# Performance work log

Measured on AMD Instinct MI355X. Metric: run time of the kernel, lower is better.

The kernel has to match this reference:

```python
import jax, jax.numpy as jnp
import numpy as np

B, S, D, HD, H = 4, 4096, 1024, 120, 1  # batch, seq, d_model, h_dim, heads (code only runs for h=1)
EPS = 1e-12  # F.normalize eps


def setup_inputs() -> dict:
    key = jax.random.key(0)
    k0, k1, k2, k3 = jax.random.split(key, 4)
    query = jax.random.normal(k0, (B, S, D), dtype=jnp.float32)
    key_t = jax.random.normal(k1, (B, S, D), dtype=jnp.float32)  # unused by forward, but a required arg
    # q_linear: Linear(d_model, h_dim*h) -> weight [HD, D], bias [HD]
    Wq = jax.random.normal(k2, (HD * H, D), dtype=jnp.float32) * np.float32(1.0 / np.sqrt(D))
    bq = jnp.zeros((HD * H,), dtype=jnp.float32)
    # weight_tensor: xavier_uniform on shape (h, d_k) = (1, 120)
    bound = np.float32(np.sqrt(6.0 / (H + HD * H)))
    weight_tensor = jax.random.uniform(k3, (H, HD * H), dtype=jnp.float32, minval=-bound, maxval=bound)
    return {"query": query, "key": key_t, "Wq": Wq, "bq": bq, "weight_tensor": weight_tensor}


def reference(query, key, Wq, bq, weight_tensor):
    # context = q_linear(query).view(B, -1, h_dim); with h=1 this is [B, S, HD]
    context = jnp.einsum('bsd,hd->bsh', query, Wq) + bq  # [B,S,HD]
    # context_fc = context.unsqueeze(0) * weight_tensor[h,1,1,d_k] -> [h,B,S,HD]
    ctx = context[None, :, :, :] * weight_tensor[:, None, None, :]  # [h,B,S,HD]
    # F.normalize(p=2, dim=-1): x / max(||x||, eps)
    nrm = jnp.sqrt(jnp.sum(ctx * ctx, axis=-1, keepdims=True))
    ctx_n = ctx / jnp.maximum(nrm, EPS)
    # per-head gram matrix then mean over heads -> [B,S,S]
    scores = jnp.einsum('hbsd,hbtd->hbst', ctx_n, ctx_n).mean(axis=0)
    # mask=None path; dropout is identity in eval mode
    return jax.nn.softmax(scores, axis=-1)
```

## Files before the change

kernel.cpp:

```cpp
#include <hip/hip_runtime.h>
#include <hip/hip_fp16.h>

#define BATCH   4
#define SEQ     4096
#define DMODEL  1024
#define HDIM    120
#define ROWS_TOTAL (BATCH * SEQ)
#define TPB     256

typedef float f32x4 __attribute__((ext_vector_type(4)));
typedef short s16x8 __attribute__((ext_vector_type(8)));

#define FRAG_PER_B ((size_t)TPB * 4 * 64)

static __device__ __forceinline__ unsigned short f2bf(float f) {
    unsigned u = __float_as_uint(f);
    u += 0x7FFFu + ((u >> 16) & 1u);
    return (unsigned short)(u >> 16);
}
static __device__ __forceinline__ s16x8 pack2x4(f32x4 lo, f32x4 hi) {
    s16x8 r;
#pragma unroll
    for (int i = 0; i < 4; ++i) r[i] = (short)f2bf(lo[i]);
#pragma unroll
    for (int i = 0; i < 4; ++i) r[4 + i] = (short)f2bf(hi[i]);
    return r;
}

__global__ __launch_bounds__(64)
void wq_frag_kernel(const float* __restrict__ Wq, const float* __restrict__ wt,
                    s16x8* __restrict__ WF)
{
    const int lane = threadIdx.x;
    const int l15  = lane & 15;
    const int l4   = lane >> 4;
    const int ct   = blockIdx.x >> 5;
    const int ks   = blockIdx.x & 31;
    const int col  = ct * 16 + l15;

    f32x4 lo = (f32x4){0.f,0.f,0.f,0.f}, hi = lo;
    if (col < HDIM) {
        const float w = wt[col];
        const float* src = Wq + (size_t)col * DMODEL + ks * 32 + l4 * 8;
        lo = *(const f32x4*)(src);
        hi = *(const f32x4*)(src + 4);
#pragma unroll
        for (int i = 0; i < 4; ++i) { lo[i] *= w; hi[i] *= w; }
    }
    WF[((size_t)(ct * 32 + ks)) * 64 + lane] = pack2x4(lo, hi);
}

__global__ __launch_bounds__(512)
void ctx_norm_kernel(const float* __restrict__ query,
                     const s16x8* __restrict__ WF,
                     const float* __restrict__ bq,
                     const float* __restrict__ wt,
                     s16x8* __restrict__ F)
{
    __shared__ unsigned short lA[2][64 * 40];
    __shared__ float lsq[64][2];
    __shared__ unsigned short lt[64][136];

    const int tid  = threadIdx.x;
    const int lane = tid & 63;
    const int wv   = tid >> 6;
    const int wr   = wv & 3;
    const int wc   = wv >> 2;
    const int l15  = lane & 15;
    const int l4   = lane >> 4;
    const int row0 = blockIdx.x * 64;

    const int arow = tid >> 3, achk = tid & 7;
    const float* aload = query + (size_t)(row0 + arow) * DMODEL + achk * 4;

    f32x4 acc[4];
#pragma unroll
    for (int n = 0; n < 4; ++n) acc[n] = (f32x4){0.f,0.f,0.f,0.f};

    f32x4 pr = *(const f32x4*)(aload);
    {
        const unsigned u0 = (unsigned)f2bf(pr[0]) | ((unsigned)f2bf(pr[1]) << 16);
        const unsigned u1 = (unsigned)f2bf(pr[2]) | ((unsigned)f2bf(pr[3]) << 16);
        *(uint2*)&lA[0][arow * 40 + achk * 4] = make_uint2(u0, u1);
    }

    for (int ks = 0; ks < 32; ++ks) {
        __syncthreads();
        if (ks + 1 < 32) pr = *(const f32x4*)(aload + (ks + 1) * 32);
        const int buf = ks & 1;
        const s16x8 a = *(const s16x8*)&lA[buf][(wr * 16 + l15) * 40 + l4 * 8];
#pragma unroll
        for (int n = 0; n < 4; ++n) {
            const s16x8 bfr = WF[((size_t)((wc * 4 + n) * 32 + ks)) * 64 + lane];
            acc[n] = __builtin_amdgcn_mfma_f32_16x16x32_bf16(a, bfr, acc[n], 0, 0, 0);
        }
        if (ks + 1 < 32) {
            const unsigned u0 = (unsigned)f2bf(pr[0]) | ((unsigned)f2bf(pr[1]) << 16);
            const unsigned u1 = (unsigned)f2bf(pr[2]) | ((unsigned)f2bf(pr[3]) << 16);
            *(uint2*)&lA[buf ^ 1][arow * 40 + achk * 4] = make_uint2(u0, u1);
        }
    }

    float sumsq[4] = {0.f,0.f,0.f,0.f};
#pragma unroll
    for (int n = 0; n < 4; ++n) {
        const int col = wc * 64 + n * 16 + l15;
        const float bqv = (col < HDIM) ? bq[col] * wt[col] : 0.f;
#pragma unroll
        for (int r = 0; r < 4; ++r) {
            const float v = acc[n][r] + bqv;
            acc[n][r] = v;
            sumsq[r] += v * v;
        }
    }
#pragma unroll
    for (int r = 0; r < 4; ++r) {
        float s = sumsq[r];
        s += __shfl_xor(s, 1);
        s += __shfl_xor(s, 2);
        s += __shfl_xor(s, 4);
        s += __shfl_xor(s, 8);
        sumsq[r] = s;
    }
    if (l15 == 0) {
#pragma unroll
        for (int r = 0; r < 4; ++r)
            lsq[wr * 16 + l4 * 4 + r][wc] = sumsq[r];
    }
    __syncthreads();
#pragma unroll
    for (int r = 0; r < 4; ++r) {
        const int lr = wr * 16 + l4 * 4 + r;
        const float s = lsq[lr][0] + lsq[lr][1];
        const float rinv = 1.f / fmaxf(sqrtf(s), 1e-12f);
#pragma unroll
        for (int n = 0; n < 4; ++n)
            lt[lr][wc * 64 + n * 16 + l15] = f2bf(acc[n][r] * rinv);
    }
    __syncthreads();
#pragma unroll
    for (int q = 0; q < 2; ++q) {
        const int idx = wv * 2 + q;
        const int tl  = idx >> 2;
        const int k4  = idx & 3;
        const s16x8 fr = *(const s16x8*)&lt[tl * 16 + l15][k4 * 32 + l4 * 8];
        F[((size_t)(blockIdx.x * 4 + tl) * 4 + k4) * 64 + lane] = fr;
    }
}

#define LOADT5(dst, t) { const s16x8* _p = base + (size_t)(t) * 2048;          \
    dst[0] = _p[0]; dst[1] = _p[64]; dst[2] = _p[128]; dst[3] = _p[192]; }

#define COMPT5(src, t) { f32x4 _a = (f32x4){0.f, 0.f, 0.f, 0.f};               \
    _a = __builtin_amdgcn_mfma_f32_16x16x32_bf16(src[0], rfrag[0], _a, 0,0,0); \
    _a = __builtin_amdgcn_mfma_f32_16x16x32_bf16(src[1], rfrag[1], _a, 0,0,0); \
    _a = __builtin_amdgcn_mfma_f32_16x16x32_bf16(src[2], rfrag[2], _a, 0,0,0); \
    _a = __builtin_amdgcn_mfma_f32_16x16x32_bf16(src[3], rfrag[3], _a, 0,0,0); \
    const float _e0 = __expf(_a[0]), _e1 = __expf(_a[1]);                      \
    const float _e2 = __expf(_a[2]), _e3 = __expf(_a[3]);                      \
    rs += (_e0 + _e1) + (_e2 + _e3);                                           \
    const __half2 _h01 = __floats2half2_rn(_e0, _e1);                          \
    const __half2 _h23 = __floats2half2_rn(_e2, _e3);                          \
    ex0[t] = *(const unsigned*)&_h01;                                          \
    ex1[t] = *(const unsigned*)&_h23; }

__global__ __launch_bounds__(512, 4)
void gram_fused_kernel(const s16x8* __restrict__ F, float* __restrict__ out)
{
    __shared__ unsigned short lsB[16 * 1024];
    __shared__ float lsum[16][8];

    const int tid  = threadIdx.x;
    const int lane = tid & 63;
    const int cg   = tid >> 6;
    const int l15  = lane & 15;
    const int l4   = lane >> 4;
    char* lsb = (char*)&lsB[0];

    const int u    = ((blockIdx.x & 7) << 7) | (blockIdx.x >> 3);
    const int b    = u >> 8;
    const int tr   = u & 255;
    const s16x8* Fb = F + (size_t)b * FRAG_PER_B;

    s16x8 rfrag[4];
#pragma unroll
    for (int ks = 0; ks < 4; ++ks) rfrag[ks] = Fb[((size_t)tr * 4 + ks) * 64 + lane];

    const s16x8* base = Fb + (size_t)cg * 256 + lane;

    unsigned ex0[32], ex1[32];
    float rs = 0.f;
    s16x8 cf[4];

#pragma unroll
    for (int t = 0; t < 32; ++t) {
        LOADT5(cf, t)
        COMPT5(cf, t)
    }

    rs += __shfl_xor(rs, 16);
    rs += __shfl_xor(rs, 32);
    if (lane < 16) lsum[lane][cg] = rs;
    __syncthreads();

    const int r0 = cg * 2, r1 = cg * 2 + 1;
    float s0 = 0.f, s1 = 0.f;
#pragma unroll
    for (int w = 0; w < 8; ++w) { s0 += lsum[r0][w]; s1 += lsum[r1][w]; }
    const float rv0 = 1.f / s0;
    const float rv1 = 1.f / s1;

    float* ob0 = out + ((size_t)b * SEQ + tr * 16 + r0) * SEQ;
    float* ob1 = out + ((size_t)b * SEQ + tr * 16 + r1) * SEQ;
    const unsigned wswz = (unsigned)((l15 & 7) << 4);
    const unsigned rswz0 = (unsigned)((r0 & 7) << 4);
    const unsigned rswz1 = (unsigned)((r1 & 7) << 4);

#pragma unroll
    for (int c = 0; c < 4; ++c) {
        if (c > 0) __syncthreads();
#pragma unroll
        for (int i = 0; i < 8; ++i) {
            const int t = c * 8 + i;
            const unsigned byte = ((unsigned)(l15 * 2048 + (i * 8 + cg) * 32 + l4 * 8)) ^ wswz;
            *(uint2*)(lsb + byte) = make_uint2(ex0[t], ex1[t]);
        }
        __syncthreads();
#pragma unroll
        for (int it = 0; it < 4; ++it) {
            const unsigned byA = ((unsigned)(r0 * 2048 + it * 512 + lane * 8)) ^ rswz0;
            const uint2 dA = *(const uint2*)(lsb + byA);
            const float2 a01 = __half22float2(*(const __half2*)&dA.x);
            const float2 a23 = __half22float2(*(const __half2*)&dA.y);
            f32x4 pA;
            pA[0] = a01.x * rv0; pA[1] = a01.y * rv0;
            pA[2] = a23.x * rv0; pA[3] = a23.y * rv0;
            __builtin_nontemporal_store(pA, (f32x4*)(ob0 + c * 1024 + it * 256 + lane * 4));

            const unsigned byB = ((unsigned)(r1 * 2048 + it * 512 + lane * 8)) ^ rswz1;
            const uint2 dB = *(const uint2*)(lsb + byB);
            const float2 b01 = __half22float2(*(const __half2*)&dB.x);
            const float2 b23 = __half22float2(*(const __half2*)&dB.y);
            f32x4 pB;
            pB[0] = b01.x * rv1; pB[1] = b01.y * rv1;
            pB[2] = b23.x * rv1; pB[3] = b23.y * rv1;
            __builtin_nontemporal_store(pB, (f32x4*)(ob1 + c * 1024 + it * 256 + lane * 4));
        }
    }
}

extern "C" void kernel_launch(void* const* d_in, const int* in_sizes, int n_in,
                              void* d_out, int out_size, void* d_ws, size_t ws_size,
                              hipStream_t stream)
{
    const float* query = (const float*)d_in[0];
    const float* Wq    = (const float*)d_in[2];
    const float* bq    = (const float*)d_in[3];
    const float* wt    = (const float*)d_in[4];
    float* out = (float*)d_out;
    s16x8* F  = (s16x8*)d_ws;
    s16x8* WF = (s16x8*)((char*)d_ws + (size_t)4 * 1024 * 1024);

    wq_frag_kernel<<<dim3(256), dim3(64), 0, stream>>>(Wq, wt, WF);
    ctx_norm_kernel<<<dim3(ROWS_TOTAL / 64), dim3(512), 0, stream>>>(query, WF, bq, wt, F);
    gram_fused_kernel<<<dim3(BATCH * TPB), dim3(512), 0, stream>>>(F, out);
}
```

Measured before the change: 120.1 us.

## Split fused gram-softmax into rowsum pass and double-buffered recompute-and-stream pass

The single fused kernel, which held all exponentials in registers before writing, is replaced by two kernels. The first computes row sums of exp(scores) for 32-row groups and stores the reciprocals. The second recomputes the gram tiles with MFMA and exponentiates them into a double-buffered LDS staging area, overlapping the next chunk's compute with the current chunk's nontemporal output stores. The aim is to cut register pressure and overlap compute with the dominant output write, at the cost of computing the gram matrix twice, one extra launch, and larger LDS use per block.

```diff
diff --git a/kernel.cpp b/kernel.cpp
--- a/kernel.cpp
+++ b/kernel.cpp
@@ -148,88 +148,139 @@
     }
 }
 
-#define LOADT5(dst, t) { const s16x8* _p = base + (size_t)(t) * 2048;          \
-    dst[0] = _p[0]; dst[1] = _p[64]; dst[2] = _p[128]; dst[3] = _p[192]; }
-
-#define COMPT5(src, t) { f32x4 _a = (f32x4){0.f, 0.f, 0.f, 0.f};               \
-    _a = __builtin_amdgcn_mfma_f32_16x16x32_bf16(src[0], rfrag[0], _a, 0,0,0); \
-    _a = __builtin_amdgcn_mfma_f32_16x16x32_bf16(src[1], rfrag[1], _a, 0,0,0); \
-    _a = __builtin_amdgcn_mfma_f32_16x16x32_bf16(src[2], rfrag[2], _a, 0,0,0); \
-    _a = __builtin_amdgcn_mfma_f32_16x16x32_bf16(src[3], rfrag[3], _a, 0,0,0); \
-    const float _e0 = __expf(_a[0]), _e1 = __expf(_a[1]);                      \
-    const float _e2 = __expf(_a[2]), _e3 = __expf(_a[3]);                      \
-    rs += (_e0 + _e1) + (_e2 + _e3);                                           \
-    const __half2 _h01 = __floats2half2_rn(_e0, _e1);                          \
-    const __half2 _h23 = __floats2half2_rn(_e2, _e3);                          \
-    ex0[t] = *(const unsigned*)&_h01;                                          \
-    ex1[t] = *(const unsigned*)&_h23; }
-
 __global__ __launch_bounds__(512, 4)
-void gram_fused_kernel(const s16x8* __restrict__ F, float* __restrict__ out)
-{
-    __shared__ unsigned short lsB[16 * 1024];
-    __shared__ float lsum[16][8];
+void rowsum_kernel(const s16x8* __restrict__ F, float* __restrict__ rinv)
+{
+    __shared__ float lsum[32][8];
 
     const int tid  = threadIdx.x;
     const int lane = tid & 63;
     const int cg   = tid >> 6;
     const int l15  = lane & 15;
+
+    const int u    = ((blockIdx.x & 7) << 6) | (blockIdx.x >> 3);
+    const int b    = u >> 7;
+    const int rg   = u & 127;
+    const s16x8* Fb = F + (size_t)b * FRAG_PER_B;
+
+    s16x8 rfA[4], rfB[4];
+#pragma unroll
+    for (int ks = 0; ks < 4; ++ks) {
+        rfA[ks] = Fb[((size_t)(rg * 2) * 4 + ks) * 64 + lane];
+        rfB[ks] = Fb[((size_t)(rg * 2 + 1) * 4 + ks) * 64 + lane];
+    }
+
+    const s16x8* base = Fb + (size_t)(cg * 32) * 256 + lane;
+    float rsA = 0.f, rsB = 0.f;
+
+    s16x8 cf0[4], cf1[4];
+    auto loadC = [&](s16x8* cf, int t) {
+        const s16x8* p = base + (size_t)t * 256;
+#pragma unroll
+        for (int ks = 0; ks < 4; ++ks) cf[ks] = p[ks * 64];
+    };
+    auto accum = [&](const s16x8* cf) {
+        f32x4 aA = (f32x4){0.f,0.f,0.f,0.f};
+        f32x4 aB = (f32x4){0.f,0.f,0.f,0.f};
+#pragma unroll
+        for (int ks = 0; ks < 4; ++ks) {
+            aA = __builtin_amdgcn_mfma_f32_16x16x32_bf16(cf[ks], rfA[ks], aA, 0, 0, 0);
+            aB = __builtin_amdgcn_mfma_f32_16x16x32_bf16(cf[ks], rfB[ks], aB, 0, 0, 0);
+        }
+#pragma unroll
+        for (int j = 0; j < 4; ++j) {
+            rsA += __expf(aA[j]);
+            rsB += __expf(aB[j]);
+        }
+    };
+
+    loadC(cf0, 0);
+    loadC(cf1, 1);
+    for (int t = 0; t < 32; t += 2) {
+        accum(cf0);
+        if (t + 2 < 32) loadC(cf0, t + 2);
+        accum(cf1);
+        if (t + 3 < 32) loadC(cf1, t + 3);
+    }
+
+    rsA += __shfl_xor(rsA, 16);
+    rsA += __shfl_xor(rsA, 32);
+    rsB += __shfl_xor(rsB, 16);
+    rsB += __shfl_xor(rsB, 32);
+    if (lane < 16) {
+        lsum[l15][cg]      = rsA;
+        lsum[16 + l15][cg] = rsB;
+    }
+    __syncthreads();
+    if (tid < 32) {
+        float s = 0.f;
+#pragma unroll
+        for (int w = 0; w < 8; ++w) s += lsum[tid][w];
+        rinv[(b * 128 + rg) * 32 + tid] = 1.f / s;
+    }
+}
+
+__global__ __launch_bounds__(1024, 4)
+void write_stream_kernel(const s16x8* __restrict__ F,
+                         const float* __restrict__ rinv,
+                         float* __restrict__ out)
+{
+    __shared__ unsigned short lsb[2][32 * 1024];
+
+    const int tid  = threadIdx.x;
+    const int lane = tid & 63;
+    const int w    = tid >> 6;
+    const int rt   = w >> 3;
+    const int cs   = w & 7;
+    const int l15  = lane & 15;
     const int l4   = lane >> 4;
-    char* lsb = (char*)&lsB[0];
-
-    const int u    = ((blockIdx.x & 7) << 7) | (blockIdx.x >> 3);
-    const int b    = u >> 8;
-    const int tr   = u & 255;
+
+    const int u    = ((blockIdx.x & 7) << 6) | (blockIdx.x >> 3);
+    const int b    = u >> 7;
+    const int rg   = u & 127;
     const s16x8* Fb = F + (size_t)b * FRAG_PER_B;
 
     s16x8 rfrag[4];
 #pragma unroll
-    for (int ks = 0; ks < 4; ++ks) rfrag[ks] = Fb[((size_t)tr * 4 + ks) * 64 + lane];
-
-    const s16x8* base = Fb + (size_t)cg * 256 + lane;
-
-    unsigned ex0[32], ex1[32];
-    float rs = 0.f;
-    s16x8 cf[4];
-
-#pragma unroll
-    for (int t = 0; t < 32; ++t) {
-        LOADT5(cf, t)
-        COMPT5(cf, t)
-    }
-
-    rs += __shfl_xor(rs, 16);
-    rs += __shfl_xor(rs, 32);
-    if (lane < 16) lsum[lane][cg] = rs;
-    __syncthreads();
-
-    const int r0 = cg * 2, r1 = cg * 2 + 1;
-    float s0 = 0.f, s1 = 0.f;
-#pragma unroll
-    for (int w = 0; w < 8; ++w) { s0 += lsum[r0][w]; s1 += lsum[r1][w]; }
-    const float rv0 = 1.f / s0;
-    const float rv1 = 1.f / s1;
-
-    float* ob0 = out + ((size_t)b * SEQ + tr * 16 + r0) * SEQ;
-    float* ob1 = out + ((size_t)b * SEQ + tr * 16 + r1) * SEQ;
-    const unsigned wswz = (unsigned)((l15 & 7) << 4);
-    const unsigned rswz0 = (unsigned)((r0 & 7) << 4);
-    const unsigned rswz1 = (unsigned)((r1 & 7) << 4);
-
-#pragma unroll
-    for (int c = 0; c < 4; ++c) {
-        if (c > 0) __syncthreads();
+    for (int ks = 0; ks < 4; ++ks)
+        rfrag[ks] = Fb[((size_t)(rg * 2 + rt) * 4 + ks) * 64 + lane];
+
+    const int r0 = 2 * w, r1 = 2 * w + 1;
+    const float rv0 = rinv[(b * 128 + rg) * 32 + r0];
+    const float rv1 = rinv[(b * 128 + rg) * 32 + r1];
+    float* ob0 = out + ((size_t)b * SEQ + rg * 32 + r0) * SEQ;
+    float* ob1 = out + ((size_t)b * SEQ + rg * 32 + r1) * SEQ;
+
+    const int  drow  = rt * 16 + l15;
+    const unsigned dswz = (unsigned)((drow & 7) << 4);
+    const unsigned sswz0 = (unsigned)((r0 & 7) << 4);
+    const unsigned sswz1 = (unsigned)((r1 & 7) << 4);
+
+    auto dump = [&](int c, int buf) {
+        char* lb = (char*)&lsb[buf][0];
 #pragma unroll
         for (int i = 0; i < 8; ++i) {
-            const int t = c * 8 + i;
-            const unsigned byte = ((unsigned)(l15 * 2048 + (i * 8 + cg) * 32 + l4 * 8)) ^ wswz;
-            *(uint2*)(lsb + byte) = make_uint2(ex0[t], ex1[t]);
-        }
-        __syncthreads();
+            const int tc = c * 64 + cs * 8 + i;
+            const s16x8* p = Fb + (size_t)tc * 256 + lane;
+            s16x8 cf[4];
+#pragma unroll
+            for (int ks = 0; ks < 4; ++ks) cf[ks] = p[ks * 64];
+            f32x4 a = (f32x4){0.f,0.f,0.f,0.f};
+#pragma unroll
+            for (int ks = 0; ks < 4; ++ks)
+                a = __builtin_amdgcn_mfma_f32_16x16x32_bf16(cf[ks], rfrag[ks], a, 0, 0, 0);
+            const __half2 h01 = __floats2half2_rn(__expf(a[0]), __expf(a[1]));
+            const __half2 h23 = __floats2half2_rn(__expf(a[2]), __expf(a[3]));
+            const unsigned byte = ((unsigned)(drow * 2048 + (cs * 8 + i) * 32 + l4 * 8)) ^ dswz;
+            *(uint2*)(lb + byte) = make_uint2(*(const unsigned*)&h01, *(const unsigned*)&h23);
+        }
+    };
+    auto storeph = [&](int c, int buf) {
+        const char* lb = (const char*)&lsb[buf][0];
 #pragma unroll
         for (int it = 0; it < 4; ++it) {
-            const unsigned byA = ((unsigned)(r0 * 2048 + it * 512 + lane * 8)) ^ rswz0;
-            const uint2 dA = *(const uint2*)(lsb + byA);
+            const unsigned byA = ((unsigned)(r0 * 2048 + it * 512 + lane * 8)) ^ sswz0;
+            const uint2 dA = *(const uint2*)(lb + byA);
             const float2 a01 = __half22float2(*(const __half2*)&dA.x);
             const float2 a23 = __half22float2(*(const __half2*)&dA.y);
             f32x4 pA;
@@ -237,8 +288,8 @@
             pA[2] = a23.x * rv0; pA[3] = a23.y * rv0;
             __builtin_nontemporal_store(pA, (f32x4*)(ob0 + c * 1024 + it * 256 + lane * 4));
 
-            const unsigned byB = ((unsigned)(r1 * 2048 + it * 512 + lane * 8)) ^ rswz1;
-            const uint2 dB = *(const uint2*)(lsb + byB);
+            const unsigned byB = ((unsigned)(r1 * 2048 + it * 512 + lane * 8)) ^ sswz1;
+            const uint2 dB = *(const uint2*)(lb + byB);
             const float2 b01 = __half22float2(*(const __half2*)&dB.x);
             const float2 b23 = __half22float2(*(const __half2*)&dB.y);
             f32x4 pB;
@@ -246,6 +297,15 @@
             pB[2] = b23.x * rv1; pB[3] = b23.y * rv1;
             __builtin_nontemporal_store(pB, (f32x4*)(ob1 + c * 1024 + it * 256 + lane * 4));
         }
+    };
+
+    dump(0, 0);
+    __syncthreads();
+#pragma unroll
+    for (int c = 0; c < 4; ++c) {
+        if (c < 3) dump(c + 1, (c + 1) & 1);
+        storeph(c, c & 1);
+        if (c < 3) __syncthreads();
     }
 }
 
@@ -258,10 +318,12 @@
     const float* bq    = (const float*)d_in[3];
     const float* wt    = (const float*)d_in[4];
     float* out = (float*)d_out;
-    s16x8* F  = (s16x8*)d_ws;
-    s16x8* WF = (s16x8*)((char*)d_ws + (size_t)4 * 1024 * 1024);
+    s16x8* F    = (s16x8*)d_ws;
+    s16x8* WF   = (s16x8*)((char*)d_ws + (size_t)4 * 1024 * 1024);
+    float* rinv = (float*)((char*)d_ws + (size_t)4 * 1024 * 1024 + 256 * 1024);
 
     wq_frag_kernel<<<dim3(256), dim3(64), 0, stream>>>(Wq, wt, WF);
     ctx_norm_kernel<<<dim3(ROWS_TOTAL / 64), dim3(512), 0, stream>>>(query, WF, bq, wt, F);
-    gram_fused_kernel<<<dim3(BATCH * TPB), dim3(512), 0, stream>>>(F, out);
-}
+    rowsum_kernel<<<dim3(512), dim3(512), 0, stream>>>(F, rinv);
+    write_stream_kernel<<<dim3(512), dim3(1024), 0, stream>>>(F, rinv, out);
+}
```

Measured after the change: 117.1 us. -2.5%, faster.
